# Kernel optimization log

Measured on AMD Instinct MI355X. Metric: run time of the kernel, lower is better.

Reference implementation:

```python
import jax, jax.numpy as jnp
import numpy as np

N_NODES = 100000
N_EDGES = 1600000
MIN_NORM = 1e-15
BALL_EPS = 1e-5  # stay strictly inside the unit ball


def _norm(x):
    return jnp.linalg.norm(x, axis=-1, keepdims=True)


def artanh(x):
    return jnp.arctanh(jnp.clip(x, -1.0 + BALL_EPS, 1.0 - BALL_EPS))


def proj(x):
    n = jnp.maximum(_norm(x), MIN_NORM)
    maxn = 1.0 - BALL_EPS
    return jnp.where(n > maxn, x / n * maxn, x)


def expmap0(u):
    n = jnp.maximum(_norm(u), MIN_NORM)
    return jnp.tanh(n) * u / n


def logmap0(x):
    n = jnp.maximum(_norm(x), MIN_NORM)
    return artanh(n) * x / n


def mobius_add(x, y):
    x2 = jnp.sum(x * x, -1, keepdims=True)
    y2 = jnp.sum(y * y, -1, keepdims=True)
    xy = jnp.sum(x * y, -1, keepdims=True)
    num = (1.0 + 2.0 * xy + y2) * x + (1.0 - x2) * y
    den = 1.0 + 2.0 * xy + x2 * y2
    return num / jnp.maximum(den, MIN_NORM)


def mobius_matvec(W, x):
    mx = x @ W.T
    xn = jnp.maximum(_norm(x), MIN_NORM)
    mxn = jnp.maximum(_norm(mx), MIN_NORM)
    return jnp.tanh(mxn / xn * artanh(xn)) * mx / mxn


def hyp_layer(x, W, b, edge_index, use_act, use_agg):
    h = proj(mobius_matvec(W, x))
    h = proj(mobius_add(h, expmap0(b)[None, :]))
    if use_agg:
        src, dst = edge_index[0], edge_index[1]
        t = logmap0(h)                       # tangent space at origin
        msg = t[src]                         # [E, d] gather
        agg = jax.ops.segment_sum(msg, dst, num_segments=N_NODES)
        deg = jax.ops.segment_sum(jnp.ones((edge_index.shape[1],), t.dtype),
                                  dst, num_segments=N_NODES)
        agg = agg / jnp.maximum(deg, 1.0)[:, None]   # mean aggregation
        h = proj(expmap0(agg))
    if use_act:
        h = proj(expmap0(jax.nn.relu(logmap0(h))))
    return h


def lorentz_to_poincare(x):
    return x[:, 1:] / (x[:, :1] + 1.0)


def setup_inputs() -> dict:
    key = jax.random.key(0)
    ks = jax.random.split(key, 16)
    d_in, h1, d_out = 64, 64, 32
    # valid hyperboloid points: x0 = sqrt(1 + |xs|^2)
    xs = 0.1 * jax.random.normal(ks[0], (N_NODES, d_in - 1), jnp.float32)
    x0 = jnp.sqrt(1.0 + jnp.sum(xs * xs, -1, keepdims=True))
    x = jnp.concatenate([x0, xs], axis=-1)
    edge_index = jax.random.randint(ks[1], (2, N_EDGES), 0, N_NODES, jnp.int64)

    def lin(k, o, i):
        return jax.random.normal(k, (o, i), jnp.float32) * (1.0 / np.sqrt(i))

    return {
        "x": x,
        "W1": lin(ks[2], h1, d_in - 1), "b1": jnp.zeros((h1,), jnp.float32),
        "W2": lin(ks[3], h1, h1),       "b2": jnp.zeros((h1,), jnp.float32),
        "W3": lin(ks[4], h1, h1),       "b3": jnp.zeros((h1,), jnp.float32),
        "W4": lin(ks[5], h1, h1),       "b4": jnp.zeros((h1,), jnp.float32),
        "W5": lin(ks[6], h1, h1),       "b5": jnp.zeros((h1,), jnp.float32),
        "W6": lin(ks[7], d_out, h1),    "b6": jnp.zeros((d_out,), jnp.float32),
        "edge_index": edge_index,
    }


def reference(x, W1, b1, W2, b2, W3, b3, W4, b4, W5, b5, W6, b6, edge_index):
    h = proj(lorentz_to_poincare(x))
    h = hyp_layer(h, W1, b1, edge_index, use_act=True,  use_agg=False)  # hconv1
    h = hyp_layer(h, W2, b2, edge_index, use_act=True,  use_agg=False)  # hconv_2
    h = hyp_layer(h, W3, b3, edge_index, use_act=True,  use_agg=False)  # hconv_3
    h = hyp_layer(h, W4, b4, edge_index, use_act=True,  use_agg=True)   # hconv2
    h = hyp_layer(h, W5, b5, edge_index, use_act=True,  use_agg=True)   # hconv3
    h = hyp_layer(h, W6, b6, edge_index, use_act=False, use_agg=False)  # hconv4
    return h
```

## Files before the change

### kernel.cpp

```cpp
#include <hip/hip_runtime.h>
#include <hip/hip_fp16.h>

#define NN 100000
#define NE 1600000
#define TILES 6250
#define MIN_NORM 1e-15f
#define BALL_EPS 1e-5f
#define MAXN (1.0f - BALL_EPS)
#define ZMAX 6.1030338f

#define BSH 9
#define NB 196
#define CH 8192
#define MAXB 16384

typedef __attribute__((ext_vector_type(8))) short bf16x8;
typedef __attribute__((ext_vector_type(4))) short short4v;
typedef __attribute__((ext_vector_type(4))) float f32x4;


__device__ __forceinline__ float rcpf(float x) { return __builtin_amdgcn_rcpf(x); }

__device__ __forceinline__ float ftanh(float x) {
    float e = __expf(-2.0f * x);
    return (1.0f - e) * rcpf(1.0f + e);
}

__device__ __forceinline__ float fatanh_c(float x) {
    x = fminf(fmaxf(x, -MAXN), MAXN);
    return 0.5f * __logf((1.0f + x) * rcpf(1.0f - x));
}

__device__ __forceinline__ void bsplit(float v, short& hi, short& lo) {
    unsigned u = __float_as_uint(v);
    hi = (short)(u >> 16);
    float r = v - __uint_as_float(u & 0xFFFF0000u);
    lo = (short)(__float_as_uint(r) >> 16);
}


__device__ __forceinline__ float wred(float x) {
    int t;
    t = __builtin_amdgcn_update_dpp(0, __float_as_int(x), 0x111, 0xf, 0xf, false);
    x += __int_as_float(t);
    t = __builtin_amdgcn_update_dpp(0, __float_as_int(x), 0x112, 0xf, 0xf, false);
    x += __int_as_float(t);
    t = __builtin_amdgcn_update_dpp(0, __float_as_int(x), 0x114, 0xf, 0xf, false);
    x += __int_as_float(t);
    t = __builtin_amdgcn_update_dpp(0, __float_as_int(x), 0x118, 0xf, 0xf, false);
    x += __int_as_float(t);
    t = __builtin_amdgcn_update_dpp(0, __float_as_int(x), 0x142, 0xa, 0xf, false);
    x += __int_as_float(t);
    t = __builtin_amdgcn_update_dpp(0, __float_as_int(x), 0x143, 0xc, 0xf, false);
    x += __int_as_float(t);
    return __int_as_float(__builtin_amdgcn_readlane(__float_as_int(x), 63));
}

__device__ __forceinline__ float red16(float x) {
    int t;
    t = __builtin_amdgcn_update_dpp(0, __float_as_int(x), 0xB1, 0xf, 0xf, false);
    x += __int_as_float(t);
    t = __builtin_amdgcn_update_dpp(0, __float_as_int(x), 0x4E, 0xf, 0xf, false);
    x += __int_as_float(t);
    t = __builtin_amdgcn_ds_swizzle(__float_as_int(x), 0x101F);
    x += __int_as_float(t);
    t = __builtin_amdgcn_ds_swizzle(__float_as_int(x), 0x201F);
    x += __int_as_float(t);
    return x;
}


__global__ __launch_bounds__(256) void prep_w(const float* __restrict__ W1,
                                              const float* __restrict__ W2,
                                              const float* __restrict__ W3,
                                              const float* __restrict__ W4,
                                              const float* __restrict__ W5,
                                              const float* __restrict__ W6,
                                              short* __restrict__ wsplit) {
    int m = blockIdx.y;
    const float* Ws[6] = {W1, W2, W3, W4, W5, W6};
    const int dins[6] = {63, 64, 64, 64, 64, 64};
    const int douts[6] = {64, 64, 64, 64, 64, 32};
    const float* W = Ws[m];
    int din = dins[m], dout = douts[m];
    int idx = blockIdx.x * 256 + threadIdx.x;
    int j = idx >> 6, k = idx & 63;
    float x = (j < dout && k < din) ? W[j * din + k] : 0.0f;
    short hi, lo;
    bsplit(x, hi, lo);
    wsplit[m * 8192 + idx] = hi;
    wsplit[m * 8192 + 4096 + idx] = lo;
}


__global__ __launch_bounds__(256) void l2p_kernel(const float* __restrict__ x,
                                                  short* __restrict__ outHi,
                                                  short* __restrict__ outLo,
                                                  float2* __restrict__ outNrm) {
    int lane = threadIdx.x & 63;
    int gw = blockIdx.x * (blockDim.x >> 6) + (threadIdx.x >> 6);
    int nw = gridDim.x * (blockDim.x >> 6);
    for (int node = gw; node < NN; node += nw) {
        float x0 = x[node * 64];
        float p = 0.0f;
        if (lane < 63) p = x[node * 64 + 1 + lane] * rcpf(x0 + 1.0f);
        float n = fmaxf(sqrtf(wred(p * p)), MIN_NORM);
        if (n > MAXN) p = p * (MAXN * rcpf(n));
        short hi, lo;
        bsplit(p, hi, lo);
        outHi[node * 64 + lane] = hi;
        outLo[node * 64 + lane] = lo;
        if (lane == 0) {
            float xn = fminf(n, MAXN);
            outNrm[node] = make_float2(xn, fatanh_c(xn));
        }
    }
}

template <int MODE, int NT>
__global__ __launch_bounds__(256, 3) void layer_mfma(const short* __restrict__ inHi,
                                                     const short* __restrict__ inLo,
                                                     const float2* __restrict__ inNrm,
                                                     const short* __restrict__ wsp,
                                                     const float* __restrict__ b,
                                                     short* __restrict__ outHi,
                                                     short* __restrict__ outLo,
                                                     float2* __restrict__ outNrm,
                                                     __half* __restrict__ outT,
                                                     float* __restrict__ outF) {
    const int dout = NT * 16;
    int tid = threadIdx.x;
    int lane = tid & 63;
    int q = lane >> 4;
    int m15 = lane & 15;
    int wv = (blockIdx.x * 256 + tid) >> 6;
    int nwave = (gridDim.x * 256) >> 6;

    bf16x8 wb1[NT][2], wb2[NT][2];
#pragma unroll
    for (int t = 0; t < NT; ++t)
#pragma unroll
        for (int s = 0; s < 2; ++s) {
            int off = (16 * t + m15) * 64 + 32 * s + 8 * q;
            wb1[t][s] = *(const bf16x8*)(wsp + off);
            wb2[t][s] = *(const bf16x8*)(wsp + 4096 + off);
        }

    float bv[NT], bp = 0.0f;
#pragma unroll
    for (int t = 0; t < NT; ++t) {
        bv[t] = b[16 * t + m15];
        bp = fmaf(bv[t], bv[t], bp);
    }
    float bsum = red16(bp);
    bool bnz = (bsum > 0.0f);
    float ybt[NT] = {}; float y2 = 0.0f;
    if (bnz) {
        float bn = fmaxf(sqrtf(bsum), MIN_NORM);
        float fy = ftanh(bn) * rcpf(bn);
#pragma unroll
        for (int t = 0; t < NT; ++t) ybt[t] = fy * bv[t];
        y2 = fy * fy * bsum;
    }

    for (int tt = wv; tt < TILES; tt += nwave) {
        int base = tt * 16;
        int rowoff = (base + m15) * 64;

        bf16x8 a1[2], a2[2];
#pragma unroll
        for (int s = 0; s < 2; ++s) {
            a1[s] = *(const bf16x8*)(inHi + rowoff + 32 * s + 8 * q);
            a2[s] = *(const bf16x8*)(inLo + rowoff + 32 * s + 8 * q);
        }
        float2 nrm = inNrm[base + m15];

        f32x4 acc[NT];
#pragma unroll
        for (int t = 0; t < NT; ++t) acc[t] = (f32x4){0.f, 0.f, 0.f, 0.f};
#pragma unroll
        for (int t = 0; t < NT; ++t)
#pragma unroll
            for (int s = 0; s < 2; ++s) {
                acc[t] = __builtin_amdgcn_mfma_f32_16x16x32_bf16(a1[s], wb1[t][s], acc[t], 0, 0, 0);
                acc[t] = __builtin_amdgcn_mfma_f32_16x16x32_bf16(a1[s], wb2[t][s], acc[t], 0, 0, 0);
                acc[t] = __builtin_amdgcn_mfma_f32_16x16x32_bf16(a2[s], wb1[t][s], acc[t], 0, 0, 0);
            }

        float sm[4];
#pragma unroll
        for (int r = 0; r < 4; ++r) {
            float p = 0.0f;
#pragma unroll
            for (int t = 0; t < NT; ++t) p = fmaf(acc[t][r], acc[t][r], p);
            sm[r] = red16(p);
        }

#pragma unroll
        for (int r = 0; r < 4; ++r) {
            int nd = base + 4 * q + r;
            float xn = __shfl(nrm.x, 4 * q + r);
            float axn = __shfl(nrm.y, 4 * q + r);
            float mxn = fmaxf(sqrtf(sm[r]), MIN_NORM);
            float z = mxn * rcpf(xn) * axn;
            float az = fminf(z, ZMAX);

            if (!bnz) {
                if (MODE == 2) {
                    float e = __expf(-2.0f * z);
                    float s1c = fminf((1.0f - e) * rcpf(1.0f + e), MAXN);
                    float fr = s1c * rcpf(mxn);
#pragma unroll
                    for (int t = 0; t < NT; ++t)
                        outF[(size_t)nd * dout + 16 * t + m15] = acc[t][r] * fr;
                } else {
                    float tfac = az * rcpf(mxn);
                    if (MODE == 1) {
#pragma unroll
                        for (int t = 0; t < NT; ++t)
                            outT[(size_t)nd * 64 + 16 * t + m15] = __float2half(tfac * acc[t][r]);
                    } else {
                        float tv[NT], tp = 0.0f;
#pragma unroll
                        for (int t = 0; t < NT; ++t) {
                            tv[t] = fmaxf(tfac * acc[t][r], 0.0f);
                            tp = fmaf(tv[t], tv[t], tp);
                        }
                        float tn = fmaxf(sqrtf(red16(tp)), MIN_NORM);
                        float e2 = __expf(-2.0f * tn);
                        float s2c = fminf((1.0f - e2) * rcpf(1.0f + e2), MAXN);
                        float g = s2c * rcpf(tn);
#pragma unroll
                        for (int t = 0; t < NT; ++t) {
                            short hi, lo;
                            bsplit(tv[t] * g, hi, lo);
                            int idx = nd * 64 + 16 * t + m15;
                            outHi[idx] = hi;
                            outLo[idx] = lo;
                        }
                        if (m15 == 0)
                            outNrm[nd] = make_float2(fmaxf(s2c, MIN_NORM), fminf(tn, ZMAX));
                    }
                }
            } else {
                float e = __expf(-2.0f * z);
                float s1c = fminf((1.0f - e) * rcpf(1.0f + e), MAXN);
                float fr = s1c * rcpf(mxn);
                float hv[NT];
#pragma unroll
                for (int t = 0; t < NT; ++t) hv[t] = acc[t][r] * fr;
                float hp = 0.0f;
#pragma unroll
                for (int t = 0; t < NT; ++t) hp = fmaf(hv[t], ybt[t], hp);
                float hy = red16(hp);
                float h2 = s1c * s1c;
                float den = fmaxf(1.0f + 2.0f * hy + h2 * y2, MIN_NORM);
                float rd = rcpf(den);
                float cA = (1.0f + 2.0f * hy + y2) * rd;
                float cB = (1.0f - h2) * rd;
                float hq = 0.0f;
#pragma unroll
                for (int t = 0; t < NT; ++t) {
                    hv[t] = cA * hv[t] + cB * ybt[t];
                    hq = fmaf(hv[t], hv[t], hq);
                }
                float hn = fmaxf(sqrtf(red16(hq)), MIN_NORM);
                if (MODE == 2) {
                    float f2 = fminf(hn, MAXN) * rcpf(hn);
#pragma unroll
                    for (int t = 0; t < NT; ++t)
                        outF[(size_t)nd * dout + 16 * t + m15] = hv[t] * f2;
                } else {
                    float tf = fatanh_c(fminf(hn, MAXN)) * rcpf(hn);
                    if (MODE == 1) {
#pragma unroll
                        for (int t = 0; t < NT; ++t)
                            outT[(size_t)nd * 64 + 16 * t + m15] = __float2half(tf * hv[t]);
                    } else {
                        float tv[NT], tp = 0.0f;
#pragma unroll
                        for (int t = 0; t < NT; ++t) {
                            tv[t] = fmaxf(tf * hv[t], 0.0f);
                            tp = fmaf(tv[t], tv[t], tp);
                        }
                        float tn = fmaxf(sqrtf(red16(tp)), MIN_NORM);
                        float s2c = fminf(ftanh(tn), MAXN);
                        float g = s2c * rcpf(tn);
#pragma unroll
                        for (int t = 0; t < NT; ++t) {
                            short hi, lo;
                            bsplit(tv[t] * g, hi, lo);
                            int idx = nd * 64 + 16 * t + m15;
                            outHi[idx] = hi;
                            outLo[idx] = lo;
                        }
                        if (m15 == 0)
                            outNrm[nd] = make_float2(fmaxf(s2c, MIN_NORM), fminf(tn, ZMAX));
                    }
                }
            }
        }
    }
}


__global__ __launch_bounds__(256) void p0_hist(const int* __restrict__ ei,
                                               int* __restrict__ ghist) {
    __shared__ int h[NB];
    for (int i = threadIdx.x; i < NB; i += 256) h[i] = 0;
    __syncthreads();
    int stride = gridDim.x * 256;
    for (int e = blockIdx.x * 256 + threadIdx.x; e < NE; e += stride)
        atomicAdd(&h[ei[NE + e] >> BSH], 1);
    __syncthreads();
    for (int i = threadIdx.x; i < NB; i += 256)
        if (h[i]) atomicAdd(&ghist[i], h[i]);
}

__global__ __launch_bounds__(256) void p_scan(const int* __restrict__ ghist,
                                              int* __restrict__ boff,
                                              int* __restrict__ bcur,
                                              int* __restrict__ rowptr) {
    __shared__ int lds[256];
    int t = threadIdx.x;
    int v = (t < NB) ? ghist[t] : 0;
    lds[t] = v;
    __syncthreads();
    for (int off = 1; off < 256; off <<= 1) {
        int u = (t >= off) ? lds[t - off] : 0;
        __syncthreads();
        lds[t] += u;
        __syncthreads();
    }
    if (t < NB) { boff[t] = lds[t] - v; bcur[t] = lds[t] - v; }
    if (t == NB - 1) boff[NB] = lds[t];
    if (t == 0) rowptr[NN] = NE;
}

__global__ __launch_bounds__(256) void p1_part(const int* __restrict__ ei,
                                               int* __restrict__ bcur,
                                               unsigned* __restrict__ packed) {
    __shared__ int hist[NB], excl[NB], cur[NB], gbase[NB];
    __shared__ int scan[256];
    __shared__ unsigned buf[CH];
    __shared__ unsigned char bseg[CH];
    int t = threadIdx.x;
    int e0 = blockIdx.x * CH;
    int n = min(CH, NE - e0);

    for (int i = t; i < NB; i += 256) hist[i] = 0;
    __syncthreads();
    for (int i = t; i < n; i += 256)
        atomicAdd(&hist[ei[NE + e0 + i] >> BSH], 1);
    __syncthreads();
    int v = (t < NB) ? hist[t] : 0;
    scan[t] = v;
    __syncthreads();
    for (int off = 1; off < 256; off <<= 1) {
        int u = (t >= off) ? scan[t - off] : 0;
        __syncthreads();
        scan[t] += u;
        __syncthreads();
    }
    if (t < NB) {
        excl[t] = scan[t] - v;
        cur[t] = scan[t] - v;
        gbase[t] = v ? atomicAdd(&bcur[t], v) : 0;
    }
    __syncthreads();
    for (int i = t; i < n; i += 256) {
        int src = ei[e0 + i], dst = ei[NE + e0 + i];
        int b = dst >> BSH;
        int p = atomicAdd(&cur[b], 1);
        buf[p] = ((unsigned)(dst & 511) << 17) | (unsigned)src;
        bseg[p] = (unsigned char)b;
    }
    __syncthreads();
    for (int i = t; i < n; i += 256) {
        int b = bseg[i];
        packed[gbase[b] + (i - excl[b])] = buf[i];
    }
}

__global__ __launch_bounds__(512) void p2_csr(const unsigned* __restrict__ packed,
                                              const int* __restrict__ boff,
                                              int* __restrict__ rowptr,
                                              int* __restrict__ csr) {
    __shared__ int lh[512], lex[512], lcur[512], scan[512];
    __shared__ int image[MAXB];
    int t = threadIdx.x;
    int b = blockIdx.x;
    int n0 = b << BSH;
    int nn = min(512, NN - n0);
    int ebeg = boff[b], eend = boff[b + 1];
    int cnt = eend - ebeg;

    lh[t] = 0;
    __syncthreads();
    for (int i = t; i < cnt; i += 512)
        atomicAdd(&lh[packed[ebeg + i] >> 17], 1);
    __syncthreads();
    int v = lh[t];
    scan[t] = v;
    __syncthreads();
    for (int off = 1; off < 512; off <<= 1) {
        int u = (t >= off) ? scan[t - off] : 0;
        __syncthreads();
        scan[t] += u;
        __syncthreads();
    }
    lex[t] = scan[t] - v;
    lcur[t] = scan[t] - v;
    if (t < nn) rowptr[n0 + t] = ebeg + lex[t];
    __syncthreads();
    for (int i = t; i < cnt; i += 512) {
        unsigned p = packed[ebeg + i];
        int pos = atomicAdd(&lcur[p >> 17], 1);
        image[pos] = (int)(p & 0x1FFFFu);
    }
    __syncthreads();
    for (int i = t; i < cnt; i += 512)
        csr[ebeg + i] = image[i];
}


__global__ __launch_bounds__(256) void gather_post_kernel(const __half* __restrict__ t16,
                                                          const int* __restrict__ rowptr,
                                                          const int* __restrict__ csr,
                                                          short* __restrict__ outHi,
                                                          short* __restrict__ outLo,
                                                          float2* __restrict__ outNrm) {
    int lane = threadIdx.x & 63;
    int g = lane >> 4;
    int l16 = lane & 15;
    int dq = l16 << 2;
    int gw = blockIdx.x * (blockDim.x >> 6) + (threadIdx.x >> 6);
    int nw = gridDim.x * (blockDim.x >> 6);
    for (int node = gw; node < NN; node += nw) {
        int beg = __builtin_amdgcn_readfirstlane(rowptr[node]);
        int end = __builtin_amdgcn_readfirstlane(rowptr[node + 1]);
        float ax = 0.f, ay = 0.f, az = 0.f, aw = 0.f;
        float bx = 0.f, by = 0.f, bz = 0.f, bw = 0.f;
        int i = beg;
        for (; i + 8 <= end; i += 8) {
            int sA = csr[i + g];
            int sB = csr[i + 4 + g];
            uint2 uA = *(const uint2*)(t16 + ((sA << 6) + dq));
            uint2 uB = *(const uint2*)(t16 + ((sB << 6) + dq));
            float2 fA0 = __half22float2(*(const half2*)&uA.x);
            float2 fA1 = __half22float2(*(const half2*)&uA.y);
            float2 fB0 = __half22float2(*(const half2*)&uB.x);
            float2 fB1 = __half22float2(*(const half2*)&uB.y);
            ax += fA0.x; ay += fA0.y; az += fA1.x; aw += fA1.y;
            bx += fB0.x; by += fB0.y; bz += fB1.x; bw += fB1.y;
        }
        for (; i < end; i += 4) {
            int idx = i + g;
            if (idx < end) {
                int s = csr[idx];
                uint2 u = *(const uint2*)(t16 + ((s << 6) + dq));
                float2 f0 = __half22float2(*(const half2*)&u.x);
                float2 f1 = __half22float2(*(const half2*)&u.y);
                ax += f0.x; ay += f0.y; az += f1.x; aw += f1.y;
            }
        }
        ax += bx; ay += by; az += bz; aw += bw;
        ax += __shfl_xor(ax, 16); ax += __shfl_xor(ax, 32);
        ay += __shfl_xor(ay, 16); ay += __shfl_xor(ay, 32);
        az += __shfl_xor(az, 16); az += __shfl_xor(az, 32);
        aw += __shfl_xor(aw, 16); aw += __shfl_xor(aw, 32);
        float rdeg = rcpf(fmaxf((float)(end - beg), 1.0f));
        ax *= rdeg; ay *= rdeg; az *= rdeg; aw *= rdeg;

        float p = fmaf(ax, ax, fmaf(ay, ay, fmaf(az, az, aw * aw)));
        p = red16(p);
        float n = fmaxf(sqrtf(p), MIN_NORM);
        float c = (n > ZMAX) ? (ZMAX * rcpf(n)) : 1.0f;
        float tx = fmaxf(c * ax, 0.f), ty = fmaxf(c * ay, 0.f);
        float tz = fmaxf(c * az, 0.f), tw = fmaxf(c * aw, 0.f);
        float tp = fmaf(tx, tx, fmaf(ty, ty, fmaf(tz, tz, tw * tw)));
        tp = red16(tp);
        float tn = fmaxf(sqrtf(tp), MIN_NORM);
        float e2 = __expf(-2.0f * tn);
        float s2c = fminf((1.0f - e2) * rcpf(1.0f + e2), MAXN);
        float g2 = s2c * rcpf(tn);
        if (g == 0) {
            float o[4] = {tx * g2, ty * g2, tz * g2, tw * g2};
            short4v hi, lo;
#pragma unroll
            for (int j = 0; j < 4; ++j) { short h, l; bsplit(o[j], h, l); hi[j] = h; lo[j] = l; }
            *(short4v*)(outHi + node * 64 + dq) = hi;
            *(short4v*)(outLo + node * 64 + dq) = lo;
            if (l16 == 0)
                outNrm[node] = make_float2(fmaxf(s2c, MIN_NORM), fminf(tn, ZMAX));
        }
    }
}


extern "C" void kernel_launch(void* const* d_in, const int* in_sizes, int n_in,
                              void* d_out, int out_size, void* d_ws, size_t ws_size,
                              hipStream_t stream) {
    const float* x  = (const float*)d_in[0];
    const float* W1 = (const float*)d_in[1];  const float* b1 = (const float*)d_in[2];
    const float* W2 = (const float*)d_in[3];  const float* b2 = (const float*)d_in[4];
    const float* W3 = (const float*)d_in[5];  const float* b3 = (const float*)d_in[6];
    const float* W4 = (const float*)d_in[7];  const float* b4 = (const float*)d_in[8];
    const float* W5 = (const float*)d_in[9];  const float* b5 = (const float*)d_in[10];
    const float* W6 = (const float*)d_in[11]; const float* b6 = (const float*)d_in[12];
    const int*   ei = (const int*)d_in[13];
    float* out = (float*)d_out;

    char* w = (char*)d_ws;
    short*   AHi  = (short*)w;            w += (size_t)NN * 64 * 2;
    short*   ALo  = (short*)w;            w += (size_t)NN * 64 * 2;
    short*   BHi  = (short*)w;            w += (size_t)NN * 64 * 2;
    short*   BLo  = (short*)w;            w += (size_t)NN * 64 * 2;
    float2*  Anrm = (float2*)w;           w += (size_t)NN * 8;
    float2*  Bnrm = (float2*)w;           w += (size_t)NN * 8;
    __half*  T16  = (__half*)w;           w += (size_t)NN * 64 * 2;
    unsigned* packed = (unsigned*)T16;
    int*     csr    = (int*)w;            w += (size_t)NE * 4;
    int*     rowptr = (int*)w;            w += (size_t)(NN + 1) * 4;
    int*     ghist  = (int*)w;            w += NB * 4;
    int*     boff   = (int*)w;            w += (NB + 1) * 4;
    int*     bcur   = (int*)w;            w += NB * 4;
    short*   wsplit = (short*)w;

    dim3 blk(256);
    const int lg = 768;
    const int ng = 1024;
    const int gg = 2048;
    const int p1g = (NE + CH - 1) / CH;

    prep_w<<<dim3(16, 6), blk, 0, stream>>>(W1, W2, W3, W4, W5, W6, wsplit);
    hipMemsetAsync(ghist, 0, NB * sizeof(int), stream);
    p0_hist<<<512, blk, 0, stream>>>(ei, ghist);
    p_scan<<<1, blk, 0, stream>>>(ghist, boff, bcur, rowptr);
    p1_part<<<p1g, blk, 0, stream>>>(ei, bcur, packed);
    p2_csr<<<NB, 512, 0, stream>>>(packed, boff, rowptr, csr);

    l2p_kernel<<<ng, blk, 0, stream>>>(x, AHi, ALo, Anrm);

    layer_mfma<0, 4><<<lg, blk, 0, stream>>>(AHi, ALo, Anrm, wsplit + 0 * 8192, b1,
                                             BHi, BLo, Bnrm, nullptr, nullptr);
    layer_mfma<0, 4><<<lg, blk, 0, stream>>>(BHi, BLo, Bnrm, wsplit + 1 * 8192, b2,
                                             AHi, ALo, Anrm, nullptr, nullptr);
    layer_mfma<0, 4><<<lg, blk, 0, stream>>>(AHi, ALo, Anrm, wsplit + 2 * 8192, b3,
                                             BHi, BLo, Bnrm, nullptr, nullptr);

    layer_mfma<1, 4><<<lg, blk, 0, stream>>>(BHi, BLo, Bnrm, wsplit + 3 * 8192, b4,
                                             nullptr, nullptr, nullptr, T16, nullptr);
    gather_post_kernel<<<gg, blk, 0, stream>>>(T16, rowptr, csr, AHi, ALo, Anrm);

    layer_mfma<1, 4><<<lg, blk, 0, stream>>>(AHi, ALo, Anrm, wsplit + 4 * 8192, b5,
                                             nullptr, nullptr, nullptr, T16, nullptr);
    gather_post_kernel<<<gg, blk, 0, stream>>>(T16, rowptr, csr, BHi, BLo, Bnrm);

    layer_mfma<2, 2><<<lg, blk, 0, stream>>>(BHi, BLo, Bnrm, wsplit + 5 * 8192, b6,
                                             nullptr, nullptr, nullptr, nullptr, out);
}
```

Before: 359.0 us.

## Stage weights in LDS for MFMA layers and interleave two nodes in gather

The MFMA layer kernel now loads the split bf16 weights into padded shared memory instead of holding them in registers. This frees registers so launch bounds can rise to 4 blocks per SM, and the grid grows to about one wave per tile. The gather kernel now processes two nodes per wave at once, giving more independent loads in flight to hide latency on the random row reads. The cost is an LDS read of the weights on every tile, a per-block weight staging step, and more accumulator registers in the gather kernel.

Measured after the change: 357.6 us. About the same (-0.4%).

```diff
diff --git a/kernel.cpp b/kernel.cpp
--- a/kernel.cpp
+++ b/kernel.cpp
@@ -13,6 +13,9 @@
 #define NB 196
 #define CH 8192
 #define MAXB 16384
+
+#define WSTRIDE 72
+#define WLO (64 * WSTRIDE)
 
 typedef __attribute__((ext_vector_type(8))) short bf16x8;
 typedef __attribute__((ext_vector_type(4))) short short4v;
@@ -118,7 +121,7 @@
 }
 
 template <int MODE, int NT>
-__global__ __launch_bounds__(256, 3) void layer_mfma(const short* __restrict__ inHi,
+__global__ __launch_bounds__(256, 4) void layer_mfma(const short* __restrict__ inHi,
                                                      const short* __restrict__ inLo,
                                                      const float2* __restrict__ inNrm,
                                                      const short* __restrict__ wsp,
@@ -129,22 +132,20 @@
                                                      __half* __restrict__ outT,
                                                      float* __restrict__ outF) {
     const int dout = NT * 16;
+    __shared__ short sW[2 * WLO];
     int tid = threadIdx.x;
+    for (int idx = tid; idx < 4096; idx += 256) {
+        int j = idx >> 6, k = idx & 63;
+        sW[j * WSTRIDE + k] = wsp[idx];
+        sW[WLO + j * WSTRIDE + k] = wsp[4096 + idx];
+    }
+    __syncthreads();
+
     int lane = tid & 63;
     int q = lane >> 4;
     int m15 = lane & 15;
     int wv = (blockIdx.x * 256 + tid) >> 6;
     int nwave = (gridDim.x * 256) >> 6;
-
-    bf16x8 wb1[NT][2], wb2[NT][2];
-#pragma unroll
-    for (int t = 0; t < NT; ++t)
-#pragma unroll
-        for (int s = 0; s < 2; ++s) {
-            int off = (16 * t + m15) * 64 + 32 * s + 8 * q;
-            wb1[t][s] = *(const bf16x8*)(wsp + off);
-            wb2[t][s] = *(const bf16x8*)(wsp + 4096 + off);
-        }
 
     float bv[NT], bp = 0.0f;
 #pragma unroll
@@ -179,13 +180,19 @@
 #pragma unroll
         for (int t = 0; t < NT; ++t) acc[t] = (f32x4){0.f, 0.f, 0.f, 0.f};
 #pragma unroll
-        for (int t = 0; t < NT; ++t)
-#pragma unroll
-            for (int s = 0; s < 2; ++s) {
-                acc[t] = __builtin_amdgcn_mfma_f32_16x16x32_bf16(a1[s], wb1[t][s], acc[t], 0, 0, 0);
-                acc[t] = __builtin_amdgcn_mfma_f32_16x16x32_bf16(a1[s], wb2[t][s], acc[t], 0, 0, 0);
-                acc[t] = __builtin_amdgcn_mfma_f32_16x16x32_bf16(a2[s], wb1[t][s], acc[t], 0, 0, 0);
-            }
+        for (int t = 0; t < NT; ++t) {
+            int woff = (16 * t + m15) * WSTRIDE + 8 * q;
+            bf16x8 w10 = *(const bf16x8*)(sW + woff);
+            bf16x8 w11 = *(const bf16x8*)(sW + woff + 32);
+            bf16x8 w20 = *(const bf16x8*)(sW + WLO + woff);
+            bf16x8 w21 = *(const bf16x8*)(sW + WLO + woff + 32);
+            acc[t] = __builtin_amdgcn_mfma_f32_16x16x32_bf16(a1[0], w10, acc[t], 0, 0, 0);
+            acc[t] = __builtin_amdgcn_mfma_f32_16x16x32_bf16(a1[1], w11, acc[t], 0, 0, 0);
+            acc[t] = __builtin_amdgcn_mfma_f32_16x16x32_bf16(a1[0], w20, acc[t], 0, 0, 0);
+            acc[t] = __builtin_amdgcn_mfma_f32_16x16x32_bf16(a1[1], w21, acc[t], 0, 0, 0);
+            acc[t] = __builtin_amdgcn_mfma_f32_16x16x32_bf16(a2[0], w10, acc[t], 0, 0, 0);
+            acc[t] = __builtin_amdgcn_mfma_f32_16x16x32_bf16(a2[1], w11, acc[t], 0, 0, 0);
+        }
 
         float sm[4];
 #pragma unroll
@@ -424,6 +431,43 @@
 }
 
 
+__device__ __forceinline__ void gp_post(float ax, float ay, float az, float aw,
+                                        int deg, int node, int l16, int g,
+                                        short* __restrict__ outHi,
+                                        short* __restrict__ outLo,
+                                        float2* __restrict__ outNrm) {
+    ax += __shfl_xor(ax, 16); ax += __shfl_xor(ax, 32);
+    ay += __shfl_xor(ay, 16); ay += __shfl_xor(ay, 32);
+    az += __shfl_xor(az, 16); az += __shfl_xor(az, 32);
+    aw += __shfl_xor(aw, 16); aw += __shfl_xor(aw, 32);
+    float rdeg = rcpf(fmaxf((float)deg, 1.0f));
+    ax *= rdeg; ay *= rdeg; az *= rdeg; aw *= rdeg;
+
+    float p = fmaf(ax, ax, fmaf(ay, ay, fmaf(az, az, aw * aw)));
+    p = red16(p);
+    float n = fmaxf(sqrtf(p), MIN_NORM);
+    float c = (n > ZMAX) ? (ZMAX * rcpf(n)) : 1.0f;
+    float tx = fmaxf(c * ax, 0.f), ty = fmaxf(c * ay, 0.f);
+    float tz = fmaxf(c * az, 0.f), tw = fmaxf(c * aw, 0.f);
+    float tp = fmaf(tx, tx, fmaf(ty, ty, fmaf(tz, tz, tw * tw)));
+    tp = red16(tp);
+    float tn = fmaxf(sqrtf(tp), MIN_NORM);
+    float e2 = __expf(-2.0f * tn);
+    float s2c = fminf((1.0f - e2) * rcpf(1.0f + e2), MAXN);
+    float g2 = s2c * rcpf(tn);
+    if (g == 0) {
+        int dq = l16 << 2;
+        float o[4] = {tx * g2, ty * g2, tz * g2, tw * g2};
+        short4v hi, lo;
+#pragma unroll
+        for (int j = 0; j < 4; ++j) { short h, l; bsplit(o[j], h, l); hi[j] = h; lo[j] = l; }
+        *(short4v*)(outHi + node * 64 + dq) = hi;
+        *(short4v*)(outLo + node * 64 + dq) = lo;
+        if (l16 == 0)
+            outNrm[node] = make_float2(fmaxf(s2c, MIN_NORM), fminf(tn, ZMAX));
+    }
+}
+
 __global__ __launch_bounds__(256) void gather_post_kernel(const __half* __restrict__ t16,
                                                           const int* __restrict__ rowptr,
                                                           const int* __restrict__ csr,
@@ -436,64 +480,86 @@
     int dq = l16 << 2;
     int gw = blockIdx.x * (blockDim.x >> 6) + (threadIdx.x >> 6);
     int nw = gridDim.x * (blockDim.x >> 6);
-    for (int node = gw; node < NN; node += nw) {
-        int beg = __builtin_amdgcn_readfirstlane(rowptr[node]);
-        int end = __builtin_amdgcn_readfirstlane(rowptr[node + 1]);
-        float ax = 0.f, ay = 0.f, az = 0.f, aw = 0.f;
-        float bx = 0.f, by = 0.f, bz = 0.f, bw = 0.f;
-        int i = beg;
-        for (; i + 8 <= end; i += 8) {
-            int sA = csr[i + g];
-            int sB = csr[i + 4 + g];
+    for (int n0 = gw; n0 < NN; n0 += 2 * nw) {
+        int n1 = n0 + nw;
+        bool has1 = (n1 < NN);
+        int b0 = __builtin_amdgcn_readfirstlane(rowptr[n0]);
+        int e0 = __builtin_amdgcn_readfirstlane(rowptr[n0 + 1]);
+        int b1 = has1 ? __builtin_amdgcn_readfirstlane(rowptr[n1]) : 0;
+        int e1 = has1 ? __builtin_amdgcn_readfirstlane(rowptr[n1 + 1]) : 0;
+
+        float ax0 = 0.f, ay0 = 0.f, az0 = 0.f, aw0 = 0.f;
+        float bx0 = 0.f, by0 = 0.f, bz0 = 0.f, bw0 = 0.f;
+        float ax1 = 0.f, ay1 = 0.f, az1 = 0.f, aw1 = 0.f;
+        float bx1 = 0.f, by1 = 0.f, bz1 = 0.f, bw1 = 0.f;
+        int i0 = b0, i1 = b1;
+
+        while (i0 + 8 <= e0 && i1 + 8 <= e1) {
+            int sA0 = csr[i0 + g], sB0 = csr[i0 + 4 + g];
+            int sA1 = csr[i1 + g], sB1 = csr[i1 + 4 + g];
+            uint2 uA0 = *(const uint2*)(t16 + ((sA0 << 6) + dq));
+            uint2 uB0 = *(const uint2*)(t16 + ((sB0 << 6) + dq));
+            uint2 uA1 = *(const uint2*)(t16 + ((sA1 << 6) + dq));
+            uint2 uB1 = *(const uint2*)(t16 + ((sB1 << 6) + dq));
+            float2 f;
+            f = __half22float2(*(const half2*)&uA0.x); ax0 += f.x; ay0 += f.y;
+            f = __half22float2(*(const half2*)&uA0.y); az0 += f.x; aw0 += f.y;
+            f = __half22float2(*(const half2*)&uB0.x); bx0 += f.x; by0 += f.y;
+            f = __half22float2(*(const half2*)&uB0.y); bz0 += f.x; bw0 += f.y;
+            f = __half22float2(*(const half2*)&uA1.x); ax1 += f.x; ay1 += f.y;
+            f = __half22float2(*(const half2*)&uA1.y); az1 += f.x; aw1 += f.y;
+            f = __half22float2(*(const half2*)&uB1.x); bx1 += f.x; by1 += f.y;
+            f = __half22float2(*(const half2*)&uB1.y); bz1 += f.x; bw1 += f.y;
+            i0 += 8; i1 += 8;
+        }
+        while (i0 + 8 <= e0) {
+            int sA = csr[i0 + g], sB = csr[i0 + 4 + g];
             uint2 uA = *(const uint2*)(t16 + ((sA << 6) + dq));
             uint2 uB = *(const uint2*)(t16 + ((sB << 6) + dq));
-            float2 fA0 = __half22float2(*(const half2*)&uA.x);
-            float2 fA1 = __half22float2(*(const half2*)&uA.y);
-            float2 fB0 = __half22float2(*(const half2*)&uB.x);
-            float2 fB1 = __half22float2(*(const half2*)&uB.y);
-            ax += fA0.x; ay += fA0.y; az += fA1.x; aw += fA1.y;
-            bx += fB0.x; by += fB0.y; bz += fB1.x; bw += fB1.y;
-        }
-        for (; i < end; i += 4) {
-            int idx = i + g;
-            if (idx < end) {
+            float2 f;
+            f = __half22float2(*(const half2*)&uA.x); ax0 += f.x; ay0 += f.y;
+            f = __half22float2(*(const half2*)&uA.y); az0 += f.x; aw0 += f.y;
+            f = __half22float2(*(const half2*)&uB.x); bx0 += f.x; by0 += f.y;
+            f = __half22float2(*(const half2*)&uB.y); bz0 += f.x; bw0 += f.y;
+            i0 += 8;
+        }
+        while (i1 + 8 <= e1) {
+            int sA = csr[i1 + g], sB = csr[i1 + 4 + g];
+            uint2 uA = *(const uint2*)(t16 + ((sA << 6) + dq));
+            uint2 uB = *(const uint2*)(t16 + ((sB << 6) + dq));
+            float2 f;
+            f = __half22float2(*(const half2*)&uA.x); ax1 += f.x; ay1 += f.y;
+            f = __half22float2(*(const half2*)&uA.y); az1 += f.x; aw1 += f.y;
+            f = __half22float2(*(const half2*)&uB.x); bx1 += f.x; by1 += f.y;
+            f = __half22float2(*(const half2*)&uB.y); bz1 += f.x; bw1 += f.y;
+            i1 += 8;
+        }
+        for (; i0 < e0; i0 += 4) {
+            int idx = i0 + g;
+            if (idx < e0) {
                 int s = csr[idx];
                 uint2 u = *(const uint2*)(t16 + ((s << 6) + dq));
                 float2 f0 = __half22float2(*(const half2*)&u.x);
                 float2 f1 = __half22float2(*(const half2*)&u.y);
-                ax += f0.x; ay += f0.y; az += f1.x; aw += f1.y;
+                ax0 += f0.x; ay0 += f0.y; az0 += f1.x; aw0 += f1.y;
             }
         }
-        ax += bx; ay += by; az += bz; aw += bw;
-        ax += __shfl_xor(ax, 16); ax += __shfl_xor(ax, 32);
-        ay += __shfl_xor(ay, 16); ay += __shfl_xor(ay, 32);
-        az += __shfl_xor(az, 16); az += __shfl_xor(az, 32);
-        aw += __shfl_xor(aw, 16); aw += __shfl_xor(aw, 32);
-        float rdeg = rcpf(fmaxf((float)(end - beg), 1.0f));
-        ax *= rdeg; ay *= rdeg; az *= rdeg; aw *= rdeg;
-
-        float p = fmaf(ax, ax, fmaf(ay, ay, fmaf(az, az, aw * aw)));
-        p = red16(p);
-        float n = fmaxf(sqrtf(p), MIN_NORM);
-        float c = (n > ZMAX) ? (ZMAX * rcpf(n)) : 1.0f;
-        float tx = fmaxf(c * ax, 0.f), ty = fmaxf(c * ay, 0.f);
-        float tz = fmaxf(c * az, 0.f), tw = fmaxf(c * aw, 0.f);
-        float tp = fmaf(tx, tx, fmaf(ty, ty, fmaf(tz, tz, tw * tw)));
-        tp = red16(tp);
-        float tn = fmaxf(sqrtf(tp), MIN_NORM);
-        float e2 = __expf(-2.0f * tn);
-        float s2c = fminf((1.0f - e2) * rcpf(1.0f + e2), MAXN);
-        float g2 = s2c * rcpf(tn);
-        if (g == 0) {
-            float o[4] = {tx * g2, ty * g2, tz * g2, tw * g2};
-            short4v hi, lo;
-#pragma unroll
-            for (int j = 0; j < 4; ++j) { short h, l; bsplit(o[j], h, l); hi[j] = h; lo[j] = l; }
-            *(short4v*)(outHi + node * 64 + dq) = hi;
-            *(short4v*)(outLo + node * 64 + dq) = lo;
-            if (l16 == 0)
-                outNrm[node] = make_float2(fmaxf(s2c, MIN_NORM), fminf(tn, ZMAX));
-        }
+        for (; i1 < e1; i1 += 4) {
+            int idx = i1 + g;
+            if (idx < e1) {
+                int s = csr[idx];
+                uint2 u = *(const uint2*)(t16 + ((s << 6) + dq));
+                float2 f0 = __half22float2(*(const half2*)&u.x);
+                float2 f1 = __half22float2(*(const half2*)&u.y);
+                ax1 += f0.x; ay1 += f0.y; az1 += f1.x; aw1 += f1.y;
+            }
+        }
+
+        gp_post(ax0 + bx0, ay0 + by0, az0 + bz0, aw0 + bw0, e0 - b0, n0, l16, g,
+                outHi, outLo, outNrm);
+        if (has1)
+            gp_post(ax1 + bx1, ay1 + by1, az1 + bz1, aw1 + bw1, e1 - b1, n1, l16, g,
+                    outHi, outLo, outNrm);
     }
 }
 
@@ -528,7 +594,7 @@
     short*   wsplit = (short*)w;
 
     dim3 blk(256);
-    const int lg = 768;
+    const int lg = 1563;
     const int ng = 1024;
     const int gg = 2048;
     const int p1g = (NE + CH - 1) / CH;
```
